# Performance work log

Hardware: AMD Instinct MI355X
Metric: run time of the kernel (lower is better)

The kernel has to match this reference:

```python
import jax, jax.numpy as jnp
import numpy as np

B, L, D, H = 2, 2048, 1024, 16
DH = D // H
NEG = -10000.0

def setup_inputs() -> dict:
    key = jax.random.key(0)
    ks = jax.random.split(key, 6)
    scale = 1.0 / np.sqrt(D)
    inp = {
        "x": jax.random.normal(ks[0], (B, L, D), dtype=jnp.float32),
        "m": jnp.ones((B, L), dtype=jnp.int32),  # 1 = valid token, 0 = padded
        "Wq": jax.random.normal(ks[1], (D, D), dtype=jnp.float32) * scale,
        "bq": jnp.zeros((D,), dtype=jnp.float32),
        "Wk": jax.random.normal(ks[2], (D, D), dtype=jnp.float32) * scale,
        "bk": jnp.zeros((D,), dtype=jnp.float32),
        "Wv": jax.random.normal(ks[3], (D, D), dtype=jnp.float32) * scale,
        "bv": jnp.zeros((D,), dtype=jnp.float32),
        "Wp": jax.random.normal(ks[4], (D, D), dtype=jnp.float32) * scale,
        "bp": jnp.zeros((D,), dtype=jnp.float32),
    }
    return inp

def reference(x, m, Wq, bq, Wk, bk, Wv, bv, Wp, bp):
    # torch Linear: x @ W.T + b
    def heads(t):  # (B,L,D) -> (B,H,L,DH)
        return t.reshape(B, L, H, DH).transpose(0, 2, 1, 3)
    q = heads(x @ Wq.T + bq)
    k = heads(x @ Wk.T + bk)
    v = heads(x @ Wv.T + bv)
    att = jnp.einsum("bhqd,bhkd->bhqk", q, k) * (1.0 / np.sqrt(DH))  # (B,H,L,L)
    causal = jnp.tril(jnp.ones((L, L), dtype=bool))[None, None]       # (1,1,L,L)
    att = jnp.where(causal, att, NEG)
    # additive key-padding mask: 0 for valid, -10000 for padded keys
    pad = (1.0 - m.astype(att.dtype))[:, None, None, :] * NEG         # (B,1,1,L)
    att = att + pad
    att = jax.nn.softmax(att, axis=-1)
    y = jnp.einsum("bhqk,bhkd->bhqd", att, v)                          # (B,H,L,DH)
    y = y.transpose(0, 2, 1, 3).reshape(B, L, D)
    return y @ Wp.T + bp
```

## Files before the change

kernel.cpp:

```cpp
#include <hip/hip_runtime.h>
#include <hip/hip_bf16.h>

#define NB 2
#define NL 2048
#define ND 1024
#define NH 16
#define NDH 64
#define NM (NB*NL)

typedef unsigned short u16;
typedef __attribute__((ext_vector_type(8))) short short8;
typedef __attribute__((ext_vector_type(4))) float floatx4;

__device__ __forceinline__ u16 f2bf(float f) {
  union { float f; unsigned int u; } v; v.f = f;
  unsigned int r = v.u + 0x7FFF + ((v.u >> 16) & 1);
  return (u16)(r >> 16);
}

__device__ __forceinline__ void async_cp16(u16* lds, const u16* g) {
  __builtin_amdgcn_global_load_lds(
      (const __attribute__((address_space(1))) void*)g,
      (__attribute__((address_space(3))) void*)lds, 16, 0, 0);
}

__device__ __forceinline__ unsigned dpp_xor1(unsigned v) {
  return (unsigned)__builtin_amdgcn_mov_dpp((int)v, 0xB1, 0xF, 0xF, true);
}

__global__ __launch_bounds__(256)
void cvt_all(const float* __restrict__ wq, const float* __restrict__ wk,
             const float* __restrict__ wv, const float* __restrict__ wp,
             const float* __restrict__ x,
             u16* __restrict__ ow, u16* __restrict__ ox)
{
  const int per4 = ND * ND / 4;
  const int tot  = 4 * per4 + NM * ND / 4;
  for (int t = blockIdx.x * 256 + threadIdx.x; t < tot; t += gridDim.x * 256) {
    const float* src; uint2* dst; int off;
    if (t < 4 * per4) {
      int w = t >> 18; off = t & (per4 - 1);
      src = (w == 0) ? wq : (w == 1) ? wk : (w == 2) ? wv : wp;
      dst = (uint2*)(ow + (size_t)w * ND * ND);
    } else {
      off = t - 4 * per4; src = x; dst = (uint2*)ox;
    }
    float4 f = ((const float4*)src)[off];
    u16 h[4] = { f2bf(f.x), f2bf(f.y), f2bf(f.z), f2bf(f.w) };
    dst[off] = *(const uint2*)h;
  }
}

#define BM 128
#define BN 128
#define BK 32
#define LDT 32

template<bool C_F32>
__global__ __launch_bounds__(256)
void gemm_bt_bias(const u16* __restrict__ A,
                  const u16* __restrict__ W0, const u16* __restrict__ W1, const u16* __restrict__ W2,
                  const float* __restrict__ B0, const float* __restrict__ B1, const float* __restrict__ B2,
                  void* __restrict__ C0, void* __restrict__ C1, void* __restrict__ C2,
                  float scale0)
{
  const int z = blockIdx.z;
  const u16* W    = (z == 0) ? W0 : (z == 1) ? W1 : W2;
  const float* Bi = (z == 0) ? B0 : (z == 1) ? B1 : B2;
  void* C         = (z == 0) ? C0 : (z == 1) ? C1 : C2;
  const float sc  = (z == 0) ? scale0 : 1.0f;

  const int n0 = blockIdx.x * BN;
  const int m0 = blockIdx.y * BM;
  const int tid  = threadIdx.x;
  const int lane = tid & 63;
  const int wave = tid >> 6;
  const int wm = (wave >> 1) * 64;
  const int wn = (wave & 1) * 64;
  const int quad = lane >> 4;
  const int l16  = lane & 15;

  __shared__ u16 As[BM * LDT];
  __shared__ u16 Bs[BN * LDT];

  floatx4 acc[4][4];
#pragma unroll
  for (int i = 0; i < 4; ++i)
#pragma unroll
    for (int j = 0; j < 4; ++j)
      acc[i][j] = (floatx4){0.f, 0.f, 0.f, 0.f};

  for (int k0 = 0; k0 < ND; k0 += BK) {
#pragma unroll
    for (int it = 0; it < 2; ++it) {
      int idx = tid + it * 256;
      int rr  = idx >> 2;
      int c8  = (idx & 3) << 3;
      async_cp16(&Bs[idx * 8], &W[(size_t)(n0 + rr) * ND + k0 + c8]);
      async_cp16(&As[idx * 8], &A[(size_t)(m0 + rr) * ND + k0 + c8]);
    }
    __syncthreads();

    short8 af[4], bfr[4];
#pragma unroll
    for (int i = 0; i < 4; ++i)
      af[i] = *(const short8*)&As[(wm + i * 16 + l16) * LDT + quad * 8];
#pragma unroll
    for (int j = 0; j < 4; ++j)
      bfr[j] = *(const short8*)&Bs[(wn + j * 16 + l16) * LDT + quad * 8];

#pragma unroll
    for (int i = 0; i < 4; ++i)
#pragma unroll
      for (int j = 0; j < 4; ++j)
        acc[i][j] = __builtin_amdgcn_mfma_f32_16x16x32_bf16(af[i], bfr[j], acc[i][j], 0, 0, 0);
    __syncthreads();
  }

#pragma unroll
  for (int j = 0; j < 4; ++j) {
    const int ncol = n0 + wn + j * 16 + l16;
    const float bv = Bi[ncol];
#pragma unroll
    for (int i = 0; i < 4; ++i) {
      const int mbase = m0 + wm + i * 16 + quad * 4;
#pragma unroll
      for (int r2 = 0; r2 < 4; ++r2) {
        float v = (acc[i][j][r2] + bv) * sc;
        if (C_F32) ((float*)C)[(size_t)(mbase + r2) * ND + ncol] = v;
        else       ((u16*)C)[(size_t)(mbase + r2) * ND + ncol] = f2bf(v);
      }
    }
  }
}

#define KC 64
#define PSTR 72

__global__ __launch_bounds__(256)
void attn_mfma(const u16* __restrict__ Q, const u16* __restrict__ K,
               const u16* __restrict__ V, const int* __restrict__ msk,
               u16* __restrict__ Y)
{
  const int t = blockIdx.x;
  const int r = t >> 8;
  const int s = t & 7;
  const int bh = (t & 255) >> 3;
  const int qt = (r == 0) ? 31 - s : (r == 1) ? 16 + s : (r == 2) ? 15 - s : s;
  const int b = bh >> 4;
  const int h = bh & 15;
  const int q0 = qt * 64;
  const int tid  = threadIdx.x;
  const int lane = tid & 63;
  const int wave = tid >> 6;
  const int wq   = wave * 16;
  const int quad = lane >> 4;
  const int l16  = lane & 15;

  __shared__ u16 Ks[KC][PSTR];
  __shared__ u16 Vt[NDH][PSTR];
  __shared__ u16 Ps[64][PSTR];
  __shared__ u16 Ms[NL];

  const int nchunks = qt + 1;

  for (int j = tid; j < nchunks * KC; j += 256) Ms[j] = (u16)(msk[b * NL + j] ? 1 : 0);

  short8 qf[2];
#pragma unroll
  for (int kk = 0; kk < 2; ++kk)
    qf[kk] = *(const short8*)&Q[(size_t)(b * NL + q0 + wq + l16) * ND
                                + h * NDH + kk * 32 + quad * 8];

  short8 onesf;
  {
    const short ov = (l16 == 0) ? (short)0x3F80 : (short)0;
#pragma unroll
    for (int e = 0; e < 8; ++e) onesf[e] = ov;
  }

  floatx4 o[4];
#pragma unroll
  for (int ot = 0; ot < 4; ++ot) o[ot] = (floatx4){0.f, 0.f, 0.f, 0.f};
  floatx4 lacc = (floatx4){0.f, 0.f, 0.f, 0.f};

  const int odd = l16 & 1;
  for (int kc = 0; kc < nchunks; ++kc) {
    const int k0 = kc * KC;

#pragma unroll
    for (int p = 0; p < 2; ++p) {
      int idx = tid + p * 256;
      int rr = idx >> 3, c = (idx & 7) << 3;
      *(uint4*)&Ks[rr][c] = *(const uint4*)&K[(size_t)(b * NL + k0 + rr) * ND + h * NDH + c];
    }
    {
      int rv = (tid & 31) * 2;
      int c  = (tid >> 5) * 8;
      uint4 va = *(const uint4*)&V[(size_t)(b * NL + k0 + rv)     * ND + h * NDH + c];
      uint4 vb = *(const uint4*)&V[(size_t)(b * NL + k0 + rv + 1) * ND + h * NDH + c];
      const u16* ap = (const u16*)&va;
      const u16* bp = (const u16*)&vb;
#pragma unroll
      for (int e = 0; e < 8; ++e)
        *(unsigned int*)&Vt[c + e][rv] = (unsigned int)ap[e] | ((unsigned int)bp[e] << 16);
    }
    __syncthreads();

    floatx4 sc[4];
#pragma unroll
    for (int ct = 0; ct < 4; ++ct) {
      short8 kf0 = *(const short8*)&Ks[ct * 16 + l16][quad * 8];
      short8 kf1 = *(const short8*)&Ks[ct * 16 + l16][32 + quad * 8];
      floatx4 a = (floatx4){0.f, 0.f, 0.f, 0.f};
      a = __builtin_amdgcn_mfma_f32_16x16x32_bf16(qf[0], kf0, a, 0, 0, 0);
      a = __builtin_amdgcn_mfma_f32_16x16x32_bf16(qf[1], kf1, a, 0, 0, 0);
      sc[ct] = a;
    }

    const bool diag = (kc == qt);
    const int rowb = q0 + wq + quad * 4;
#pragma unroll
    for (int ct = 0; ct < 4; ++ct) {
      const int col = k0 + ct * 16 + l16;
      const float pmul = (float)Ms[col];
      unsigned bb[4];
#pragma unroll
      for (int r2 = 0; r2 < 4; ++r2) {
        float p = pmul * __expf(sc[ct][r2]);
        if (diag) p = (col > rowb + r2) ? 0.f : p;
        bb[r2] = (unsigned)f2bf(p);
      }
      unsigned n0v = dpp_xor1(bb[0]), n1v = dpp_xor1(bb[1]);
      unsigned n2v = dpp_xor1(bb[2]), n3v = dpp_xor1(bb[3]);
      const int colb  = ct * 16 + (l16 & ~1);
      const int row01 = wq + quad * 4 + odd;
      unsigned d01 = odd ? (n1v | (bb[1] << 16)) : (bb[0] | (n0v << 16));
      unsigned d23 = odd ? (n3v | (bb[3] << 16)) : (bb[2] | (n2v << 16));
      *(unsigned*)&Ps[row01][colb]     = d01;
      *(unsigned*)&Ps[row01 + 2][colb] = d23;
    }

#pragma unroll
    for (int kk = 0; kk < 2; ++kk) {
      short8 pf = *(const short8*)&Ps[wq + l16][kk * 32 + quad * 8];
#pragma unroll
      for (int ot = 0; ot < 4; ++ot) {
        short8 vf = *(const short8*)&Vt[ot * 16 + l16][kk * 32 + quad * 8];
        o[ot] = __builtin_amdgcn_mfma_f32_16x16x32_bf16(pf, vf, o[ot], 0, 0, 0);
      }
      lacc = __builtin_amdgcn_mfma_f32_16x16x32_bf16(pf, onesf, lacc, 0, 0, 0);
    }
    __syncthreads();
  }

  float inv[4];
#pragma unroll
  for (int r2 = 0; r2 < 4; ++r2) {
    const float l = __shfl(lacc[r2], quad << 4);
    inv[r2] = 1.0f / l;
  }
#pragma unroll
  for (int ot = 0; ot < 4; ++ot)
#pragma unroll
    for (int r2 = 0; r2 < 4; ++r2) {
      const int row = q0 + wq + quad * 4 + r2;
      Y[(size_t)(b * NL + row) * ND + h * NDH + ot * 16 + l16] = f2bf(o[ot][r2] * inv[r2]);
    }
}

extern "C" void kernel_launch(void* const* d_in, const int* in_sizes, int n_in,
                              void* d_out, int out_size, void* d_ws, size_t ws_size,
                              hipStream_t stream) {
  const float* x  = (const float*)d_in[0];
  const int*   m  = (const int*)d_in[1];
  const float* Wq = (const float*)d_in[2];
  const float* bq = (const float*)d_in[3];
  const float* Wk = (const float*)d_in[4];
  const float* bk = (const float*)d_in[5];
  const float* Wv = (const float*)d_in[6];
  const float* bv = (const float*)d_in[7];
  const float* Wp = (const float*)d_in[8];
  const float* bp = (const float*)d_in[9];
  float* out = (float*)d_out;

  const size_t per = (size_t)NM * ND;
  u16* Qb = (u16*)d_ws;
  u16* Kb = Qb + per;
  u16* Vb = Kb + per;
  u16* Wb = Vb + per;
  u16* Yb = Qb;
  u16* xb = (u16*)d_out;

  cvt_all<<<2048, 256, 0, stream>>>(Wq, Wk, Wv, Wp, x, Wb, xb);

  dim3 gq(ND / BN, NM / BM, 3);
  gemm_bt_bias<false><<<gq, 256, 0, stream>>>(
      xb, Wb, Wb + (size_t)ND * ND, Wb + 2 * (size_t)ND * ND,
      bq, bk, bv, (void*)Qb, (void*)Kb, (void*)Vb, 0.125f);

  attn_mfma<<<1024, 256, 0, stream>>>(Qb, Kb, Vb, m, Yb);

  dim3 gp(ND / BN, NM / BM, 1);
  const u16* Wpb = Wb + 3 * (size_t)ND * ND;
  gemm_bt_bias<true><<<gp, 256, 0, stream>>>(
      Yb, Wpb, Wpb, Wpb, bp, bp, bp,
      (void*)out, (void*)out, (void*)out, 1.0f);
}
```

Baseline: 215.7 us.

## Split QKV and projection GEMMs, shrink proj tile, remap attention blocks per XCD

The templated z-indexed GEMM is replaced by a QKV GEMM that folds the three weights into one 2D grid along N, and by a separate output-projection GEMM with a 128x64 tile. The smaller tile doubles the projection's block count from 256 to 512, which fills more CUs on the 256-CU device. The attention block-to-(head, query tile) mapping is also reordered so each XCD (t&7) handles a fixed group of four heads, with mixed causal workloads across rounds. This is meant to improve L2 reuse of K/V per XCD and balance load, but it risks a worse tail if the per-XCD work becomes uneven.

```diff
diff --git a/kernel.cpp b/kernel.cpp
--- a/kernel.cpp
+++ b/kernel.cpp
@@ -56,21 +56,20 @@
 #define BK 32
 #define LDT 32
 
-template<bool C_F32>
 __global__ __launch_bounds__(256)
-void gemm_bt_bias(const u16* __restrict__ A,
-                  const u16* __restrict__ W0, const u16* __restrict__ W1, const u16* __restrict__ W2,
-                  const float* __restrict__ B0, const float* __restrict__ B1, const float* __restrict__ B2,
-                  void* __restrict__ C0, void* __restrict__ C1, void* __restrict__ C2,
-                  float scale0)
+void gemm_qkv(const u16* __restrict__ A, const u16* __restrict__ Wb,
+              const float* __restrict__ bq, const float* __restrict__ bk,
+              const float* __restrict__ bv,
+              u16* __restrict__ Qb, u16* __restrict__ Kb, u16* __restrict__ Vb)
 {
-  const int z = blockIdx.z;
-  const u16* W    = (z == 0) ? W0 : (z == 1) ? W1 : W2;
-  const float* Bi = (z == 0) ? B0 : (z == 1) ? B1 : B2;
-  void* C         = (z == 0) ? C0 : (z == 1) ? C1 : C2;
-  const float sc  = (z == 0) ? scale0 : 1.0f;
-
-  const int n0 = blockIdx.x * BN;
+  const int n0g = blockIdx.x * BN;
+  const int z   = n0g >> 10;
+  const int n0  = n0g & 1023;
+  const u16* W    = Wb + (size_t)z * ND * ND;
+  const float* Bi = (z == 0) ? bq : (z == 1) ? bk : bv;
+  u16* C          = (z == 0) ? Qb : (z == 1) ? Kb : Vb;
+  const float sc  = (z == 0) ? 0.125f : 1.0f;
+
   const int m0 = blockIdx.y * BM;
   const int tid  = threadIdx.x;
   const int lane = tid & 63;
@@ -120,16 +119,85 @@
 #pragma unroll
   for (int j = 0; j < 4; ++j) {
     const int ncol = n0 + wn + j * 16 + l16;
-    const float bv = Bi[ncol];
+    const float bv2 = Bi[ncol];
 #pragma unroll
     for (int i = 0; i < 4; ++i) {
       const int mbase = m0 + wm + i * 16 + quad * 4;
 #pragma unroll
       for (int r2 = 0; r2 < 4; ++r2) {
-        float v = (acc[i][j][r2] + bv) * sc;
-        if (C_F32) ((float*)C)[(size_t)(mbase + r2) * ND + ncol] = v;
-        else       ((u16*)C)[(size_t)(mbase + r2) * ND + ncol] = f2bf(v);
+        float v = (acc[i][j][r2] + bv2) * sc;
+        C[(size_t)(mbase + r2) * ND + ncol] = f2bf(v);
       }
+    }
+  }
+}
+
+#define BN2 64
+
+__global__ __launch_bounds__(256)
+void gemm_proj(const u16* __restrict__ A, const u16* __restrict__ W,
+               const float* __restrict__ Bi, float* __restrict__ C)
+{
+  const int n0 = blockIdx.x * BN2;
+  const int m0 = blockIdx.y * BM;
+  const int tid  = threadIdx.x;
+  const int lane = tid & 63;
+  const int wave = tid >> 6;
+  const int wm = (wave >> 1) * 64;
+  const int wn = (wave & 1) * 32;
+  const int quad = lane >> 4;
+  const int l16  = lane & 15;
+
+  __shared__ u16 As[BM * LDT];
+  __shared__ u16 Bs[BN2 * LDT];
+
+  floatx4 acc[4][2];
+#pragma unroll
+  for (int i = 0; i < 4; ++i)
+#pragma unroll
+    for (int j = 0; j < 2; ++j)
+      acc[i][j] = (floatx4){0.f, 0.f, 0.f, 0.f};
+
+  for (int k0 = 0; k0 < ND; k0 += BK) {
+#pragma unroll
+    for (int it = 0; it < 2; ++it) {
+      int idx = tid + it * 256;
+      int rr  = idx >> 2;
+      int c8  = (idx & 3) << 3;
+      async_cp16(&As[idx * 8], &A[(size_t)(m0 + rr) * ND + k0 + c8]);
+    }
+    {
+      int rr = tid >> 2, c8 = (tid & 3) << 3;
+      async_cp16(&Bs[tid * 8], &W[(size_t)(n0 + rr) * ND + k0 + c8]);
+    }
+    __syncthreads();
+
+    short8 af[4], bfr[2];
+#pragma unroll
+    for (int i = 0; i < 4; ++i)
+      af[i] = *(const short8*)&As[(wm + i * 16 + l16) * LDT + quad * 8];
+#pragma unroll
+    for (int j = 0; j < 2; ++j)
+      bfr[j] = *(const short8*)&Bs[(wn + j * 16 + l16) * LDT + quad * 8];
+
+#pragma unroll
+    for (int i = 0; i < 4; ++i)
+#pragma unroll
+      for (int j = 0; j < 2; ++j)
+        acc[i][j] = __builtin_amdgcn_mfma_f32_16x16x32_bf16(af[i], bfr[j], acc[i][j], 0, 0, 0);
+    __syncthreads();
+  }
+
+#pragma unroll
+  for (int j = 0; j < 2; ++j) {
+    const int ncol = n0 + wn + j * 16 + l16;
+    const float bv2 = Bi[ncol];
+#pragma unroll
+    for (int i = 0; i < 4; ++i) {
+      const int mbase = m0 + wm + i * 16 + quad * 4;
+#pragma unroll
+      for (int r2 = 0; r2 < 4; ++r2)
+        C[(size_t)(mbase + r2) * ND + ncol] = acc[i][j][r2] + bv2;
     }
   }
 }
@@ -144,9 +212,13 @@
 {
   const int t = blockIdx.x;
   const int r = t >> 8;
-  const int s = t & 7;
-  const int bh = (t & 255) >> 3;
-  const int qt = (r == 0) ? 31 - s : (r == 1) ? 16 + s : (r == 2) ? 15 - s : s;
+  const int xcd = t & 7;
+  const int v = (t >> 3) & 31;
+  const int bh = xcd * 4 + r;
+  const int qt = (r == 0) ? v
+               : (r == 1) ? 31 - v
+               : (r == 2) ? ((v + 16) & 31)
+                          : ((15 - v) & 31);
   const int b = bh >> 4;
   const int h = bh & 15;
   const int q0 = qt * 64;
@@ -294,16 +366,11 @@
 
   cvt_all<<<2048, 256, 0, stream>>>(Wq, Wk, Wv, Wp, x, Wb, xb);
 
-  dim3 gq(ND / BN, NM / BM, 3);
-  gemm_bt_bias<false><<<gq, 256, 0, stream>>>(
-      xb, Wb, Wb + (size_t)ND * ND, Wb + 2 * (size_t)ND * ND,
-      bq, bk, bv, (void*)Qb, (void*)Kb, (void*)Vb, 0.125f);
+  gemm_qkv<<<dim3(3 * ND / BN, NM / BM), 256, 0, stream>>>(
+      xb, Wb, bq, bk, bv, Qb, Kb, Vb);
 
   attn_mfma<<<1024, 256, 0, stream>>>(Qb, Kb, Vb, m, Yb);
 
-  dim3 gp(ND / BN, NM / BM, 1);
   const u16* Wpb = Wb + 3 * (size_t)ND * ND;
-  gemm_bt_bias<true><<<gp, 256, 0, stream>>>(
-      Yb, Wpb, Wpb, Wpb, bp, bp, bp,
-      (void*)out, (void*)out, (void*)out, 1.0f);
-}
+  gemm_proj<<<dim3(ND / BN2, NM / BM), 256, 0, stream>>>(Yb, Wpb, bp, out);
+}
```

Result: faster. 210.3 us (-2.5%).
